# Kernel tuning notes

Hardware: AMD Instinct MI355X
Metric: run time of the kernel (lower is better)

## Reference

```python
import jax, jax.numpy as jnp
import numpy as np

D_MODEL = 768
N_HEADS = 12
D_K = D_MODEL // N_HEADS


def setup_inputs() -> dict:
    key = jax.random.key(0)
    ks = jax.random.split(key, 9)
    B, S = 4, 2048
    sc = 1.0 / np.sqrt(D_MODEL)
    inp = {"x": jax.random.normal(ks[0], (B, S, D_MODEL), dtype=jnp.float32)}
    names = ["q", "k", "v", "o"]
    for i, n in enumerate(names):
        inp[f"W{n}"] = jax.random.normal(ks[1 + 2 * i], (D_MODEL, D_MODEL), dtype=jnp.float32) * sc
        inp[f"b{n}"] = jax.random.normal(ks[2 + 2 * i], (D_MODEL,), dtype=jnp.float32) * 0.01
    return inp


def reference(x, Wq, bq, Wk, bk, Wv, bv, Wo, bo):
    B, S, _ = x.shape
    def split_heads(t):  # [B,S,D] -> [B,H,S,d_k]
        return t.reshape(B, S, N_HEADS, D_K).transpose(0, 2, 1, 3)
    Q = split_heads(x @ Wq.T + bq)
    K = split_heads(x @ Wk.T + bk)
    V = split_heads(x @ Wv.T + bv)
    # NOTE: original divides by d_k, not sqrt(d_k)
    scores = jnp.einsum("bhqd,bhkd->bhqk", Q, K) / D_K
    scores = jax.nn.softmax(scores, axis=-1)
    att = jnp.einsum("bhqk,bhkd->bhqd", scores, V)  # [B,H,S,d_k]
    att = att.transpose(0, 2, 1, 3).reshape(B, S, D_MODEL)
    return att @ Wo.T + bo
```

## Files before the change

### kernel.cpp

```cpp
#include <hip/hip_runtime.h>
#include <hip/hip_bf16.h>

typedef __bf16 bf16;
typedef _Float16 f16;
typedef bf16 bf16x8 __attribute__((ext_vector_type(8)));
typedef bf16 bf16x4 __attribute__((ext_vector_type(4)));
typedef f16 f16x4 __attribute__((ext_vector_type(4)));
typedef f16 f16x2 __attribute__((ext_vector_type(2)));
typedef float f32x4 __attribute__((ext_vector_type(4)));

#define SLEN 2048
#define HEADS 12
#define DMODEL 768

#define GLOAD16(g, l) \
    __builtin_amdgcn_global_load_lds((const __attribute__((address_space(1))) void*)(g), \
                                     (__attribute__((address_space(3))) void*)(l), 16, 0, 0)

__global__ void cvt_all(const float* __restrict__ x,
                        const float* __restrict__ Wq, const float* __restrict__ Wk,
                        const float* __restrict__ Wv, const float* __restrict__ Wo,
                        bf16* __restrict__ xb, bf16* __restrict__ wdst) {
    int idx = blockIdx.x * 256 + threadIdx.x;
    const float* s; bf16* d;
    if (idx < 1572864) {
        s = x; d = xb;
    } else {
        int t = idx - 1572864;
        int wi = t / 147456;
        idx = t - wi * 147456;
        s = (wi == 0) ? Wq : (wi == 1) ? Wk : (wi == 2) ? Wv : Wo;
        d = wdst + (size_t)wi * 589824;
    }
    float4 v = ((const float4*)s)[idx];
    bf16x4 o;
    o[0] = (bf16)v.x; o[1] = (bf16)v.y; o[2] = (bf16)v.z; o[3] = (bf16)v.w;
    *(bf16x4*)(d + (size_t)idx * 4) = o;
}

__global__ __launch_bounds__(256, 2) void gemm_qkv(
    const bf16* __restrict__ A, const bf16* __restrict__ Bw,
    const float* __restrict__ bq, const float* __restrict__ bk, const float* __restrict__ bv,
    bf16* __restrict__ Qb, bf16* __restrict__ Kb, f16* __restrict__ VTb)
{
    __shared__ __align__(16) char smem[49152];
    typedef bf16 ATile[128][32];
    typedef bf16 BTile[256][32];
    ATile* As = (ATile*)smem;
    BTile* Bs = (BTile*)(smem + 16384);
    const int K = DMODEL;
    int tid = threadIdx.x;
    int w = tid >> 6, lane = tid & 63, i16 = lane & 15, q4 = lane >> 4;
    int mblk = (w & 1) * 64, nblk = (w >> 1) * 128;
    int row0 = blockIdx.y * 128, col0 = blockIdx.x * 256;
    int srow = lane >> 2, scol = (lane & 3) * 8;
    f32x4 acc[8][4] = {};

    const bf16* Ab = A  + (size_t)(row0 + w * 16 + srow) * K + scol;
    const bf16* Bb = Bw + (size_t)(col0 + w * 16 + srow) * K + scol;

#define STAGE(buf, k0) do { \
        GLOAD16(Ab + (k0),                   &As[buf][w * 16][0]); \
        GLOAD16(Ab + (size_t)64 * K + (k0),  &As[buf][w * 16 + 64][0]); \
        GLOAD16(Bb + (k0),                   &Bs[buf][w * 16][0]); \
        GLOAD16(Bb + (size_t)64 * K + (k0),  &Bs[buf][w * 16 + 64][0]); \
        GLOAD16(Bb + (size_t)128 * K + (k0), &Bs[buf][w * 16 + 128][0]); \
        GLOAD16(Bb + (size_t)192 * K + (k0), &Bs[buf][w * 16 + 192][0]); \
    } while (0)

    STAGE(0, 0);
    __syncthreads();
    int buf = 0;
    for (int k0 = 0; k0 < K; k0 += 32, buf ^= 1) {
        if (k0 + 32 < K) STAGE(buf ^ 1, k0 + 32);
        bf16x8 af[4], bfr[8];
#pragma unroll
        for (int t = 0; t < 4; ++t) af[t]  = *(const bf16x8*)(&As[buf][mblk + t * 16 + i16][q4 * 8]);
#pragma unroll
        for (int t = 0; t < 8; ++t) bfr[t] = *(const bf16x8*)(&Bs[buf][nblk + t * 16 + i16][q4 * 8]);
#pragma unroll
        for (int ct = 0; ct < 8; ++ct)
#pragma unroll
            for (int st = 0; st < 4; ++st)
                acc[ct][st] = __builtin_amdgcn_mfma_f32_16x16x32_bf16(bfr[ct], af[st], acc[ct][st], 0, 0, 0);
        __syncthreads();
    }
#undef STAGE

    int region = col0 / DMODEL;
    int cbase = col0 - region * DMODEL + nblk;

    if (region < 2) {
        const float* bias = region ? bk : bq;
        bf16* dstb = region ? Kb : Qb;
#pragma unroll
        for (int ct = 0; ct < 8; ++ct) {
#pragma unroll
            for (int st = 0; st < 4; ++st) {
                int c0 = cbase + ct * 16 + q4 * 4;
                int h = c0 >> 6, d0 = c0 & 63;
                int sg = row0 + mblk + st * 16 + i16;
                int b = sg >> 11, s = sg & 2047;
                float4 bb = *(const float4*)(bias + c0);
                bf16x4 o;
                if (region == 0) {
                    o[0] = (bf16)((acc[ct][st][0] + bb.x) * 0.0225421217f);
                    o[1] = (bf16)((acc[ct][st][1] + bb.y) * 0.0225421217f);
                    o[2] = (bf16)((acc[ct][st][2] + bb.z) * 0.0225421217f);
                    o[3] = (bf16)((acc[ct][st][3] + bb.w) * 0.0225421217f);
                } else {
                    o[0] = (bf16)(acc[ct][st][0] + bb.x);
                    o[1] = (bf16)(acc[ct][st][1] + bb.y);
                    o[2] = (bf16)(acc[ct][st][2] + bb.z);
                    o[3] = (bf16)(acc[ct][st][3] + bb.w);
                }
                *(bf16x4*)(dstb + (((size_t)(b * HEADS + h)) * SLEN + s) * 64 + d0) = o;
            }
        }
    } else {
        f16 (*Cs)[132] = (f16(*)[132])smem;
#pragma unroll
        for (int p = 0; p < 2; ++p) {
            if ((w >> 1) == p) {
#pragma unroll
                for (int ct = 0; ct < 8; ++ct) {
#pragma unroll
                    for (int st = 0; st < 4; ++st) {
                        int cg = cbase + ct * 16 + q4 * 4;
                        float4 bb = *(const float4*)(bv + cg);
                        f16x4 vv;
                        vv[0] = (f16)(acc[ct][st][0] + bb.x);
                        vv[1] = (f16)(acc[ct][st][1] + bb.y);
                        vv[2] = (f16)(acc[ct][st][2] + bb.z);
                        vv[3] = (f16)(acc[ct][st][3] + bb.w);
                        *(f16x4*)(&Cs[mblk + st * 16 + i16][ct * 16 + q4 * 4]) = vv;
                    }
                }
            }
            __syncthreads();
            int cl = lane * 2;
            int cg = (col0 - 2 * DMODEL) + p * 128 + cl;
            int h = cg >> 6, d = cg & 63;
            int s0 = w * 32;
            int b = row0 >> 11, sg = (row0 & 2047) + s0;
            f16* dst0 = VTb + ((size_t)(b * HEADS + h) * 64 + d) * SLEN + sg;
            f16* dst1 = dst0 + SLEN;
#pragma unroll
            for (int j = 0; j < 4; ++j) {
                unsigned v[8];
#pragma unroll
                for (int i = 0; i < 8; ++i) v[i] = *(const unsigned*)(&Cs[s0 + j * 8 + i][cl]);
                unsigned lo[4], hi[4];
#pragma unroll
                for (int i = 0; i < 4; ++i) {
                    lo[i] = (v[2 * i] & 0xffffu) | (v[2 * i + 1] << 16);
                    hi[i] = (v[2 * i] >> 16) | (v[2 * i + 1] & 0xffff0000u);
                }
                *(uint4*)(dst0 + j * 8) = *(uint4*)lo;
                *(uint4*)(dst1 + j * 8) = *(uint4*)hi;
            }
            __syncthreads();
        }
    }
}

__global__ __launch_bounds__(256, 3) void gemm_out(
    const bf16* __restrict__ A, const bf16* __restrict__ Bw,
    const float* __restrict__ bo, float* __restrict__ out)
{
    __shared__ bf16 As[2][128][32];
    __shared__ bf16 Bs[2][128][32];
    const int K = DMODEL;
    int tid = threadIdx.x;
    int w = tid >> 6, lane = tid & 63, i16 = lane & 15, q4 = lane >> 4;
    int mblk = (w & 1) * 64, nblk = (w >> 1) * 64;
    int row0 = blockIdx.y * 128, col0 = blockIdx.x * 128;
    int srow = (lane >> 2), scol = (lane & 3) * 8;
    f32x4 acc[4][4] = {};

    const bf16* Ab = A  + (size_t)(row0 + w * 16 + srow) * K + scol;
    const bf16* Bb = Bw + (size_t)(col0 + w * 16 + srow) * K + scol;

#define STAGE(buf, k0) do { \
        GLOAD16(Ab + (k0),                  &As[buf][w * 16][0]); \
        GLOAD16(Ab + (size_t)64 * K + (k0), &As[buf][w * 16 + 64][0]); \
        GLOAD16(Bb + (k0),                  &Bs[buf][w * 16][0]); \
        GLOAD16(Bb + (size_t)64 * K + (k0), &Bs[buf][w * 16 + 64][0]); \
    } while (0)

    STAGE(0, 0);
    __syncthreads();
    int buf = 0;
    for (int k0 = 0; k0 < K; k0 += 32, buf ^= 1) {
        if (k0 + 32 < K) STAGE(buf ^ 1, k0 + 32);
        bf16x8 af[4], bfr[4];
#pragma unroll
        for (int t = 0; t < 4; ++t) af[t] = *(const bf16x8*)(&As[buf][mblk + t * 16 + i16][q4 * 8]);
#pragma unroll
        for (int t = 0; t < 4; ++t) bfr[t] = *(const bf16x8*)(&Bs[buf][nblk + t * 16 + i16][q4 * 8]);
#pragma unroll
        for (int ct = 0; ct < 4; ++ct)
#pragma unroll
            for (int st = 0; st < 4; ++st)
                acc[ct][st] = __builtin_amdgcn_mfma_f32_16x16x32_bf16(bfr[ct], af[st], acc[ct][st], 0, 0, 0);
        __syncthreads();
    }
#undef STAGE

#pragma unroll
    for (int ct = 0; ct < 4; ++ct) {
#pragma unroll
        for (int st = 0; st < 4; ++st) {
            int c0 = col0 + nblk + ct * 16 + q4 * 4;
            int s = row0 + mblk + st * 16 + i16;
            float4 bb = *(const float4*)(bo + c0);
            float4 o = {acc[ct][st][0] + bb.x, acc[ct][st][1] + bb.y,
                        acc[ct][st][2] + bb.z, acc[ct][st][3] + bb.w};
            *(float4*)(out + (size_t)s * DMODEL + c0) = o;
        }
    }
}

__global__ __launch_bounds__(256, 3) void attn_kernel(
    const bf16* __restrict__ Qb, const bf16* __restrict__ Kb,
    const f16* __restrict__ VTb, bf16* __restrict__ att)
{
    __shared__ bf16 Ks[128][64];
    __shared__ f16  Vt[64][128];

    int tid = threadIdx.x;
    int w = tid >> 6, lane = tid & 63, i16 = lane & 15, q4 = lane >> 4;
    int qt = blockIdx.x, h = blockIdx.y, b = blockIdx.z;
    size_t bh = (size_t)b * HEADS + h;
    const bf16* Qp = Qb + (bh * SLEN + qt * 128 + w * 32) * 64;
    const bf16* Kp = Kb + bh * SLEN * 64;
    const f16*  Vp = VTb + bh * 64 * SLEN;

    bf16x8 aq[2][2];
#pragma unroll
    for (int qs = 0; qs < 2; ++qs) {
        aq[qs][0] = *(const bf16x8*)(Qp + (qs * 16 + i16) * 64 + q4 * 8);
        aq[qs][1] = *(const bf16x8*)(Qp + (qs * 16 + i16) * 64 + 32 + q4 * 8);
    }

    int rlK = lane >> 3;
    int cK = (lane & 7) ^ rlK;
    const bf16* kp[4];
#pragma unroll
    for (int j = 0; j < 4; ++j)
        kp[j] = Kp + (size_t)(w * 32 + j * 8 + rlK) * 64 + cK * 8;
    int rlV = lane >> 4;
    const f16* vp[4];
#pragma unroll
    for (int j = 0; j < 4; ++j) {
        int rowa = w * 16 + j * 4 + rlV;
        int cV = (lane & 15) ^ (rowa & 15);
        vp[j] = Vp + (size_t)rowa * SLEN + cV * 8;
    }

    f16x4 vones = {};
    if (i16 == 0) { vones[0] = (f16)1; vones[1] = (f16)1; vones[2] = (f16)1; vones[3] = (f16)1; }

    f32x4 oacc[2][4] = {};
    f32x4 lacc[2] = {};
    int ck0 = (q4 ^ (i16 & 7)) * 8;
    int ck1 = ((q4 ^ 4) ^ (i16 & 7)) * 8;
    int q4h = q4 >> 1, q4l = (q4 & 1) * 4;

    for (int kt = 0; kt < 16; ++kt) {
#pragma unroll
        for (int j = 0; j < 4; ++j) {
            GLOAD16(kp[j], &Ks[w * 32 + j * 8][0]);
            GLOAD16(vp[j], &Vt[w * 16 + j * 4][0]);
            kp[j] += 128 * 64;
            vp[j] += 128;
        }
        __syncthreads();

#pragma unroll
        for (int t = 0; t < 8; ++t) {
            bf16x8 kf0 = *(const bf16x8*)(&Ks[t * 16 + i16][ck0]);
            bf16x8 kf1 = *(const bf16x8*)(&Ks[t * 16 + i16][ck1]);
            f16x4 pf[2];
#pragma unroll
            for (int qs = 0; qs < 2; ++qs) {
                f32x4 z = {};
                z = __builtin_amdgcn_mfma_f32_16x16x32_bf16(kf0, aq[qs][0], z, 0, 0, 0);
                z = __builtin_amdgcn_mfma_f32_16x16x32_bf16(kf1, aq[qs][1], z, 0, 0, 0);
                f16x2 p01 = __builtin_bit_cast(f16x2,
                    __builtin_amdgcn_cvt_pkrtz(__builtin_amdgcn_exp2f(z[0]),
                                               __builtin_amdgcn_exp2f(z[1])));
                f16x2 p23 = __builtin_bit_cast(f16x2,
                    __builtin_amdgcn_cvt_pkrtz(__builtin_amdgcn_exp2f(z[2]),
                                               __builtin_amdgcn_exp2f(z[3])));
                pf[qs][0] = p01[0]; pf[qs][1] = p01[1];
                pf[qs][2] = p23[0]; pf[qs][3] = p23[1];
                lacc[qs] = __builtin_amdgcn_mfma_f32_16x16x16f16(vones, pf[qs], lacc[qs], 0, 0, 0);
            }
#pragma unroll
            for (int dt = 0; dt < 4; ++dt) {
                int vc = ((2 * t + q4h) ^ i16) * 8 + q4l;
                f16x4 vf = *(const f16x4*)(&Vt[dt * 16 + i16][vc]);
                oacc[0][dt] = __builtin_amdgcn_mfma_f32_16x16x16f16(vf, pf[0], oacc[0][dt], 0, 0, 0);
                oacc[1][dt] = __builtin_amdgcn_mfma_f32_16x16x16f16(vf, pf[1], oacc[1][dt], 0, 0, 0);
            }
        }
        __syncthreads();
    }

#pragma unroll
    for (int qs = 0; qs < 2; ++qs) {
        float l = __shfl(lacc[qs][0], i16);
        float inv = 1.f / l;
        int row = qt * 128 + w * 32 + qs * 16 + i16;
        size_t obase = ((size_t)b * SLEN + row) * DMODEL + h * 64;
#pragma unroll
        for (int dt = 0; dt < 4; ++dt) {
            bf16x4 o;
#pragma unroll
            for (int r = 0; r < 4; ++r) o[r] = (bf16)(oacc[qs][dt][r] * inv);
            *(bf16x4*)(att + obase + dt * 16 + q4 * 4) = o;
        }
    }
}

extern "C" void kernel_launch(void* const* d_in, const int* in_sizes, int n_in,
                              void* d_out, int out_size, void* d_ws, size_t ws_size,
                              hipStream_t stream) {
    const float* x  = (const float*)d_in[0];
    const float* Wq = (const float*)d_in[1];
    const float* bq = (const float*)d_in[2];
    const float* Wk = (const float*)d_in[3];
    const float* bk = (const float*)d_in[4];
    const float* Wv = (const float*)d_in[5];
    const float* bv = (const float*)d_in[6];
    const float* Wo = (const float*)d_in[7];
    const float* bo = (const float*)d_in[8];
    float* out = (float*)d_out;

    char* ws = (char*)d_ws;
    bf16* xb   = (bf16*)(ws);
    bf16* wqkv = (bf16*)(ws + 12582912);
    bf16* wob  = (bf16*)(ws + 16121856);
    bf16* Qb   = (bf16*)(ws + 17301504);
    bf16* Kb   = (bf16*)(ws + 29884416);
    f16*  VTb  = (f16*)(ws + 42467328);
    bf16* attb = xb;

    cvt_all<<<8448, 256, 0, stream>>>(x, Wq, Wk, Wv, Wo, xb, wqkv);
    gemm_qkv<<<dim3(9, 64), 256, 0, stream>>>(xb, wqkv, bq, bk, bv, Qb, Kb, VTb);
    attn_kernel<<<dim3(16, 12, 4), 256, 0, stream>>>(Qb, Kb, VTb, attb);
    gemm_out<<<dim3(6, 64), 256, 0, stream>>>(attb, wob, bo, out);
}
```

Measured before the change: 234.5 us.

## Use 16x16x32 f16 MFMA for PV in attention and shrink output GEMM tile

The attention kernel now computes two 16-key score tiles per step and packs 8 probabilities per lane. This lets the P·V product and the row-sum use the wider 16x16x32 f16 MFMA instead of 16x16x16. To make the packed probabilities line up with the V fragments, K rows are loaded into LDS in a permuted order. Separately, the output projection GEMM uses 128x64 tiles with twice as many blocks, aiming for better CU occupancy at the cost of more A-tile reloads.

```diff
diff --git a/kernel.cpp b/kernel.cpp
--- a/kernel.cpp
+++ b/kernel.cpp
@@ -5,6 +5,7 @@
 typedef _Float16 f16;
 typedef bf16 bf16x8 __attribute__((ext_vector_type(8)));
 typedef bf16 bf16x4 __attribute__((ext_vector_type(4)));
+typedef f16 f16x8 __attribute__((ext_vector_type(8)));
 typedef f16 f16x4 __attribute__((ext_vector_type(4)));
 typedef f16 f16x2 __attribute__((ext_vector_type(2)));
 typedef float f32x4 __attribute__((ext_vector_type(4)));
@@ -169,14 +170,13 @@
     const float* __restrict__ bo, float* __restrict__ out)
 {
     __shared__ bf16 As[2][128][32];
-    __shared__ bf16 Bs[2][128][32];
+    __shared__ bf16 Bs[2][64][32];
     const int K = DMODEL;
     int tid = threadIdx.x;
     int w = tid >> 6, lane = tid & 63, i16 = lane & 15, q4 = lane >> 4;
-    int mblk = (w & 1) * 64, nblk = (w >> 1) * 64;
-    int row0 = blockIdx.y * 128, col0 = blockIdx.x * 128;
+    int row0 = blockIdx.y * 128, col0 = blockIdx.x * 64;
     int srow = (lane >> 2), scol = (lane & 3) * 8;
-    f32x4 acc[4][4] = {};
+    f32x4 acc[4][2] = {};
 
     const bf16* Ab = A  + (size_t)(row0 + w * 16 + srow) * K + scol;
     const bf16* Bb = Bw + (size_t)(col0 + w * 16 + srow) * K + scol;
@@ -185,7 +185,6 @@
         GLOAD16(Ab + (k0),                  &As[buf][w * 16][0]); \
         GLOAD16(Ab + (size_t)64 * K + (k0), &As[buf][w * 16 + 64][0]); \
         GLOAD16(Bb + (k0),                  &Bs[buf][w * 16][0]); \
-        GLOAD16(Bb + (size_t)64 * K + (k0), &Bs[buf][w * 16 + 64][0]); \
     } while (0)
 
     STAGE(0, 0);
@@ -193,15 +192,15 @@
     int buf = 0;
     for (int k0 = 0; k0 < K; k0 += 32, buf ^= 1) {
         if (k0 + 32 < K) STAGE(buf ^ 1, k0 + 32);
-        bf16x8 af[4], bfr[4];
-#pragma unroll
-        for (int t = 0; t < 4; ++t) af[t] = *(const bf16x8*)(&As[buf][mblk + t * 16 + i16][q4 * 8]);
-#pragma unroll
-        for (int t = 0; t < 4; ++t) bfr[t] = *(const bf16x8*)(&Bs[buf][nblk + t * 16 + i16][q4 * 8]);
+        bf16x8 af[2], bfr[4];
+#pragma unroll
+        for (int t = 0; t < 2; ++t) af[t] = *(const bf16x8*)(&As[buf][w * 32 + t * 16 + i16][q4 * 8]);
+#pragma unroll
+        for (int t = 0; t < 4; ++t) bfr[t] = *(const bf16x8*)(&Bs[buf][t * 16 + i16][q4 * 8]);
 #pragma unroll
         for (int ct = 0; ct < 4; ++ct)
 #pragma unroll
-            for (int st = 0; st < 4; ++st)
+            for (int st = 0; st < 2; ++st)
                 acc[ct][st] = __builtin_amdgcn_mfma_f32_16x16x32_bf16(bfr[ct], af[st], acc[ct][st], 0, 0, 0);
         __syncthreads();
     }
@@ -210,9 +209,9 @@
 #pragma unroll
     for (int ct = 0; ct < 4; ++ct) {
 #pragma unroll
-        for (int st = 0; st < 4; ++st) {
-            int c0 = col0 + nblk + ct * 16 + q4 * 4;
-            int s = row0 + mblk + st * 16 + i16;
+        for (int st = 0; st < 2; ++st) {
+            int c0 = col0 + ct * 16 + q4 * 4;
+            int s = row0 + w * 32 + st * 16 + i16;
             float4 bb = *(const float4*)(bo + c0);
             float4 o = {acc[ct][st][0] + bb.x, acc[ct][st][1] + bb.y,
                         acc[ct][st][2] + bb.z, acc[ct][st][3] + bb.w};
@@ -247,8 +246,11 @@
     int cK = (lane & 7) ^ rlK;
     const bf16* kp[4];
 #pragma unroll
-    for (int j = 0; j < 4; ++j)
-        kp[j] = Kp + (size_t)(w * 32 + j * 8 + rlK) * 64 + cK * 8;
+    for (int j = 0; j < 4; ++j) {
+        int p = w * 32 + j * 8 + rlK;
+        int key = 32 * (p >> 5) + 8 * ((p >> 2) & 3) + 4 * ((p >> 4) & 1) + (p & 3);
+        kp[j] = Kp + (size_t)key * 64 + cK * 8;
+    }
     int rlV = lane >> 4;
     const f16* vp[4];
 #pragma unroll
@@ -258,14 +260,15 @@
         vp[j] = Vp + (size_t)rowa * SLEN + cV * 8;
     }
 
-    f16x4 vones = {};
-    if (i16 == 0) { vones[0] = (f16)1; vones[1] = (f16)1; vones[2] = (f16)1; vones[3] = (f16)1; }
+    f16x8 vones = {};
+    if (i16 == 0)
+#pragma unroll
+        for (int j = 0; j < 8; ++j) vones[j] = (f16)1;
 
     f32x4 oacc[2][4] = {};
     f32x4 lacc[2] = {};
     int ck0 = (q4 ^ (i16 & 7)) * 8;
     int ck1 = ((q4 ^ 4) ^ (i16 & 7)) * 8;
-    int q4h = q4 >> 1, q4l = (q4 & 1) * 4;
 
     for (int kt = 0; kt < 16; ++kt) {
 #pragma unroll
@@ -278,31 +281,43 @@
         __syncthreads();
 
 #pragma unroll
-        for (int t = 0; t < 8; ++t) {
-            bf16x8 kf0 = *(const bf16x8*)(&Ks[t * 16 + i16][ck0]);
-            bf16x8 kf1 = *(const bf16x8*)(&Ks[t * 16 + i16][ck1]);
-            f16x4 pf[2];
+        for (int u = 0; u < 4; ++u) {
+            bf16x8 k00 = *(const bf16x8*)(&Ks[u * 32 + i16][ck0]);
+            bf16x8 k01 = *(const bf16x8*)(&Ks[u * 32 + i16][ck1]);
+            bf16x8 k10 = *(const bf16x8*)(&Ks[u * 32 + 16 + i16][ck0]);
+            bf16x8 k11 = *(const bf16x8*)(&Ks[u * 32 + 16 + i16][ck1]);
+            f16x8 pf[2];
 #pragma unroll
             for (int qs = 0; qs < 2; ++qs) {
-                f32x4 z = {};
-                z = __builtin_amdgcn_mfma_f32_16x16x32_bf16(kf0, aq[qs][0], z, 0, 0, 0);
-                z = __builtin_amdgcn_mfma_f32_16x16x32_bf16(kf1, aq[qs][1], z, 0, 0, 0);
+                f32x4 z0 = {}, z1 = {};
+                z0 = __builtin_amdgcn_mfma_f32_16x16x32_bf16(k00, aq[qs][0], z0, 0, 0, 0);
+                z0 = __builtin_amdgcn_mfma_f32_16x16x32_bf16(k01, aq[qs][1], z0, 0, 0, 0);
+                z1 = __builtin_amdgcn_mfma_f32_16x16x32_bf16(k10, aq[qs][0], z1, 0, 0, 0);
+                z1 = __builtin_amdgcn_mfma_f32_16x16x32_bf16(k11, aq[qs][1], z1, 0, 0, 0);
                 f16x2 p01 = __builtin_bit_cast(f16x2,
-                    __builtin_amdgcn_cvt_pkrtz(__builtin_amdgcn_exp2f(z[0]),
-                                               __builtin_amdgcn_exp2f(z[1])));
+                    __builtin_amdgcn_cvt_pkrtz(__builtin_amdgcn_exp2f(z0[0]),
+                                               __builtin_amdgcn_exp2f(z0[1])));
                 f16x2 p23 = __builtin_bit_cast(f16x2,
-                    __builtin_amdgcn_cvt_pkrtz(__builtin_amdgcn_exp2f(z[2]),
-                                               __builtin_amdgcn_exp2f(z[3])));
+                    __builtin_amdgcn_cvt_pkrtz(__builtin_amdgcn_exp2f(z0[2]),
+                                               __builtin_amdgcn_exp2f(z0[3])));
+                f16x2 p45 = __builtin_bit_cast(f16x2,
+                    __builtin_amdgcn_cvt_pkrtz(__builtin_amdgcn_exp2f(z1[0]),
+                                               __builtin_amdgcn_exp2f(z1[1])));
+                f16x2 p67 = __builtin_bit_cast(f16x2,
+                    __builtin_amdgcn_cvt_pkrtz(__builtin_amdgcn_exp2f(z1[2]),
+                                               __builtin_amdgcn_exp2f(z1[3])));
                 pf[qs][0] = p01[0]; pf[qs][1] = p01[1];
                 pf[qs][2] = p23[0]; pf[qs][3] = p23[1];
-                lacc[qs] = __builtin_amdgcn_mfma_f32_16x16x16f16(vones, pf[qs], lacc[qs], 0, 0, 0);
+                pf[qs][4] = p45[0]; pf[qs][5] = p45[1];
+                pf[qs][6] = p67[0]; pf[qs][7] = p67[1];
+                lacc[qs] = __builtin_amdgcn_mfma_f32_16x16x32_f16(vones, pf[qs], lacc[qs], 0, 0, 0);
             }
 #pragma unroll
             for (int dt = 0; dt < 4; ++dt) {
-                int vc = ((2 * t + q4h) ^ i16) * 8 + q4l;
-                f16x4 vf = *(const f16x4*)(&Vt[dt * 16 + i16][vc]);
-                oacc[0][dt] = __builtin_amdgcn_mfma_f32_16x16x16f16(vf, pf[0], oacc[0][dt], 0, 0, 0);
-                oacc[1][dt] = __builtin_amdgcn_mfma_f32_16x16x16f16(vf, pf[1], oacc[1][dt], 0, 0, 0);
+                int vc = ((4 * u + q4) ^ i16) * 8;
+                f16x8 vf = *(const f16x8*)(&Vt[dt * 16 + i16][vc]);
+                oacc[0][dt] = __builtin_amdgcn_mfma_f32_16x16x32_f16(vf, pf[0], oacc[0][dt], 0, 0, 0);
+                oacc[1][dt] = __builtin_amdgcn_mfma_f32_16x16x32_f16(vf, pf[1], oacc[1][dt], 0, 0, 0);
             }
         }
         __syncthreads();
@@ -350,5 +365,5 @@
     cvt_all<<<8448, 256, 0, stream>>>(x, Wq, Wk, Wv, Wo, xb, wqkv);
     gemm_qkv<<<dim3(9, 64), 256, 0, stream>>>(xb, wqkv, bq, bk, bv, Qb, Kb, VTb);
     attn_kernel<<<dim3(16, 12, 4), 256, 0, stream>>>(Qb, Kb, VTb, attb);
-    gemm_out<<<dim3(6, 64), 256, 0, stream>>>(attb, wob, bo, out);
-}
+    gemm_out<<<dim3(12, 64), 256, 0, stream>>>(attb, wob, bo, out);
+}
```

Result: faster. 229.3 us (-2.2%).
